# Kernel optimization log

Hardware: AMD Instinct MI355X
Metric: run time of the kernel (lower is better)

Reference implementation:

```python
import math
import jax, jax.numpy as jnp
import numpy as np

B, T_BI, D_BI = 64, 3000, 128
T_SW, D_SW = 375, 192
T_S1, D_S1 = 188, 192
N_FIRES = 300          # static fire count (target_lengths all = 300 -> beta = 1, ceil(sum)=300)
D_MODEL = 512
SCALE = 4.0            # scale_factor
EPS_LN = 1e-5


def _cif_integrate(h, alpha, thr, n_fires):
    """Vectorized CIF: cumsum + two scatter-adds (matches torch _cif_forward).
    h [B,T,D], alpha [B,T], thr [B,1] -> [B,n_fires,D]."""
    Bq, T, D = h.shape
    a = alpha / thr                       # normalize so boundaries sit at integers
    c = jnp.cumsum(a, axis=1)
    prev = c - a
    kp = jnp.floor(prev)
    kc = jnp.floor(c)
    fired = kc > kp                       # frame crosses a token boundary
    w_hi = jnp.where(fired, (c - kc) * thr, 0.0)          # leftover into new token
    w_lo = jnp.where(fired, (kp + 1.0 - prev) * thr, alpha)  # portion completing old token
    ip = jnp.clip(kp.astype(jnp.int32), 0, n_fires - 1)
    ic = jnp.clip(kc.astype(jnp.int32), 0, n_fires - 1)
    bidx = jnp.broadcast_to(jnp.arange(Bq)[:, None], (Bq, T))
    out = jnp.zeros((Bq, n_fires, D), h.dtype)
    out = out.at[bidx, ip].add(w_lo[..., None] * h)
    out = out.at[bidx, ic].add(w_hi[..., None] * h)
    return out


def _interp(src, t_cont, t_bi):
    """Linear interp of src [B,Ts,D] at continuous fire times t_cont [B,N] (given on the T_bi grid)."""
    Bq, Ts, D = src.shape
    t = t_cont * Ts / t_bi
    lo = jnp.clip(t.astype(jnp.int32), 0, Ts - 2)
    w = (t - lo.astype(t.dtype))[..., None]
    idx_lo = jnp.broadcast_to(lo[..., None], (Bq, t.shape[1], D))
    g_lo = jnp.take_along_axis(src, idx_lo, axis=1)
    g_hi = jnp.take_along_axis(src, idx_lo + 1, axis=1)
    return (1.0 - w) * g_lo + w * g_hi


def _forward(fire_signal, acoustic_src, acoustic_src_s1, conv_w, ln_g, ln_b, wp_w, wp_b,
             film_s0_w, film_s0_b, film_s1_w, film_s1_b, tproj_w, tproj_b,
             aproj_w, aproj_b, bproj_w, bproj_b, target_lengths):
    Bq, T_bi, _ = fire_signal.shape
    # 1) weight predictor: depthwise conv (k=1, no bias) -> LN -> Linear -> sigmoid
    x = fire_signal * conv_w                                   # depthwise 1x1 conv
    mu = jnp.mean(x, axis=-1, keepdims=True)
    var = jnp.var(x, axis=-1, keepdims=True)
    xn = (x - mu) * jax.lax.rsqrt(var + EPS_LN) * ln_g + ln_b
    alpha = SCALE * jax.nn.sigmoid(xn @ wp_w + wp_b)           # [B,T]
    tgt = target_lengths.astype(alpha.dtype)
    qty_loss = jnp.mean(jnp.abs(jnp.sum(alpha, axis=1) - tgt))
    # training-mode alpha normalization (sum alpha_cif == target)
    sum_a = jnp.clip(jnp.sum(alpha, axis=1, keepdims=True), 1e-8)
    alpha_cif = alpha * (tgt[:, None] / sum_a)
    # dynamic threshold beta = sum / ceil(sum)  (== 1 here since targets are integers)
    sum_cif = jnp.sum(alpha_cif, axis=1)
    ceil_sum = jax.lax.stop_gradient(jnp.clip(jnp.ceil(sum_cif), 1.0))
    thr = (sum_cif / ceil_sum)[:, None]                        # [B,1]
    # 2) CIF integration of temporal channel
    acoustic_temporal = _cif_integrate(fire_signal, alpha_cif, thr, N_FIRES)  # [B,N,128]
    # continuous fire times
    cum = jnp.cumsum(alpha_cif, axis=1)
    thresholds = jnp.arange(1, N_FIRES + 1, dtype=alpha.dtype)[None, :] * thr  # [B,N]
    ff = jax.vmap(jnp.searchsorted)(cum, thresholds)
    ff = jnp.minimum(ff, T_bi - 1)
    t_lo = jnp.maximum(ff - 1, 0)
    cum_at = jnp.take_along_axis(cum, t_lo, axis=1)
    a_at = jnp.take_along_axis(alpha_cif, ff, axis=1)
    t_cont = t_lo.astype(alpha.dtype) + (thresholds - cum_at) / jnp.clip(a_at, 1e-8)
    t_cont = jnp.clip(t_cont, 0.0, T_bi - 1)
    # 3) S0 pitch channel: interp + FiLM
    acoustic_pitch = _interp(acoustic_src, t_cont, T_bi)       # [B,N,192]
    film0 = acoustic_temporal @ film_s0_w + film_s0_b
    g0, b0 = jnp.split(film0, 2, axis=-1)
    pitch_mod = g0 * acoustic_pitch + b0
    # 4) project + combine
    embs = (acoustic_temporal @ tproj_w + tproj_b) + (pitch_mod @ aproj_w + aproj_b)
    # S1 beat channel
    acoustic_beat = _interp(acoustic_src_s1, t_cont, T_bi)     # [B,N,192]
    film1 = acoustic_temporal @ film_s1_w + film_s1_b
    g1, b1 = jnp.split(film1, 2, axis=-1)
    beat_mod = g1 * acoustic_beat + b1
    embs = embs + (beat_mod @ bproj_w + bproj_b)
    return embs, alpha, qty_loss


def setup_inputs() -> dict:
    key = jax.random.key(0)
    ks = jax.random.split(key, 14)
    # weight_proj bias init per module: alpha_init = target_fires/encoder_len
    p = min((128.0 / 3000.0) / SCALE, 0.99)
    wp_bias = math.log(p / (1.0 - p))
    f32 = jnp.float32
    return {
        "fire_signal": jax.random.normal(ks[0], (B, T_BI, D_BI), f32),
        "acoustic_src": jax.random.normal(ks[1], (B, T_SW, D_SW), f32),
        "acoustic_src_s1": jax.random.normal(ks[2], (B, T_S1, D_S1), f32),
        "target_lengths": jnp.full((B,), N_FIRES, jnp.int32),
        "conv_w": 1.0 + 0.1 * jax.random.normal(ks[3], (D_BI,), f32),
        "ln_g": jnp.ones((D_BI,), f32),
        "ln_b": jnp.zeros((D_BI,), f32),
        "wp_w": 0.02 * jax.random.normal(ks[4], (D_BI,), f32),
        "wp_b": jnp.asarray(wp_bias, f32),
        "film_s0_w": 0.02 * jax.random.normal(ks[5], (D_BI, 2 * D_SW), f32),
        "film_s0_b": jnp.concatenate([jnp.ones((D_SW,), f32), jnp.zeros((D_SW,), f32)]),
        "film_s1_w": 0.02 * jax.random.normal(ks[6], (D_BI, 2 * D_S1), f32),
        "film_s1_b": jnp.concatenate([jnp.ones((D_S1,), f32), jnp.zeros((D_S1,), f32)]),
        "tproj_w": 0.02 * jax.random.normal(ks[7], (D_BI, D_MODEL), f32),
        "tproj_b": jnp.zeros((D_MODEL,), f32),
        "aproj_w": 0.02 * jax.random.normal(ks[8], (D_SW, D_MODEL), f32),
        "aproj_b": jnp.zeros((D_MODEL,), f32),
        "bproj_w": 0.02 * jax.random.normal(ks[9], (D_S1, D_MODEL), f32),
        "bproj_b": jnp.zeros((D_MODEL,), f32),
    }


def reference(fire_signal, acoustic_src, acoustic_src_s1, target_lengths, conv_w, ln_g, ln_b,
              wp_w, wp_b, film_s0_w, film_s0_b, film_s1_w, film_s1_b, tproj_w, tproj_b,
              aproj_w, aproj_b, bproj_w, bproj_b):
    return _forward(fire_signal, acoustic_src, acoustic_src_s1, conv_w, ln_g, ln_b, wp_w, wp_b,
                    film_s0_w, film_s0_b, film_s1_w, film_s1_b, tproj_w, tproj_b,
                    aproj_w, aproj_b, bproj_w, bproj_b, target_lengths)
```

## Files before the change

### kernel.cpp

```cpp
#include <hip/hip_runtime.h>
#include <math.h>

#define BQ 64
#define TBI 3000
#define DBI 128
#define TSW 375
#define TS1 188
#define DSW 192
#define NF 300
#define DMODEL 512
#define EPSLN 1e-5f

typedef __bf16 bf16x8 __attribute__((ext_vector_type(8)));
typedef float f32x4 __attribute__((ext_vector_type(4)));

__device__ __forceinline__ unsigned short f2bf(float f) {
    unsigned u = __float_as_uint(f);
    unsigned r = (u + 0x7FFFu + ((u >> 16) & 1u)) >> 16;
    return (unsigned short)r;
}

#define ALPHA_BLOCKS 24000

__global__ __launch_bounds__(256) void k_alpha_prep(
    const float* __restrict__ fs, const float* __restrict__ conv_w,
    const float* __restrict__ ln_g, const float* __restrict__ ln_b,
    const float* __restrict__ wp_w, const float* __restrict__ wp_b,
    float* __restrict__ alpha_out,
    const float* __restrict__ f0w, const float* __restrict__ f1w,
    const float* __restrict__ tw, const float* __restrict__ aw, const float* __restrict__ bw,
    const float* __restrict__ f0b, const float* __restrict__ f1b,
    const float* __restrict__ tb, const float* __restrict__ apb, const float* __restrict__ bpb,
    unsigned short* __restrict__ Wg, unsigned short* __restrict__ Wb,
    unsigned short* __restrict__ W2,
    float* __restrict__ gbias, float* __restrict__ bbias, float* __restrict__ bias2,
    float* __restrict__ qtyo)
{
    if (blockIdx.x >= ALPHA_BLOCKS) {
        int pbid = blockIdx.x - ALPHA_BLOCKS;
        if (pbid == 1216) {
            for (int c = threadIdx.x; c < 512; c += 256) {
                if (c < 384) {
                    gbias[c] = c < 192 ? f0b[c] : f1b[c - 192];
                    bbias[c] = c < 192 ? f0b[c + 192] : f1b[c - 192 + 192];
                }
                bias2[c] = tb[c] + apb[c] + bpb[c];
            }
            if (threadIdx.x == 0) qtyo[0] = 0.f;
            return;
        }
        int i = pbid * 256 + threadIdx.x;
        if (i < 49152) {
            int k = i / 384;
            int n = i - k * 384;
            float g, b;
            if (n < 192) { g = f0w[k * 384 + n]; b = f0w[k * 384 + n + 192]; }
            else         { g = f1w[k * 384 + (n - 192)]; b = f1w[k * 384 + n]; }
            int kt = k >> 5, j = k & 7;
            int lane = ((k >> 3) & 3) * 16 + (n & 15);
            int nt = n >> 4;
            int out = ((nt * 4 + kt) * 64 + lane) * 8 + j;
            Wg[out] = f2bf(g); Wb[out] = f2bf(b);
        } else {
            int ii = i - 49152;
            int k = ii >> 9, n = ii & 511;
            float v;
            if (k < 128)      v = tw[k * 512 + n];
            else if (k < 320) v = aw[(k - 128) * 512 + n];
            else              v = bw[(k - 320) * 512 + n];
            int kt = k >> 5, j = k & 7;
            int lane = ((k >> 3) & 3) * 16 + (n & 15);
            int nt = n >> 4;
            int out = ((nt * 16 + kt) * 64 + lane) * 8 + j;
            W2[out] = f2bf(v);
        }
        return;
    }
    int wave = threadIdx.x >> 6, lane = threadIdx.x & 63;
    int l = lane & 31;
    long g = (long)blockIdx.x * 8 + wave * 2 + (lane >> 5);
    const float* row = fs + g * DBI;
    float4 f  = *(const float4*)&row[4 * l];
    float4 cw = *(const float4*)&conv_w[4 * l];
    float4 x; x.x = f.x * cw.x; x.y = f.y * cw.y; x.z = f.z * cw.z; x.w = f.w * cw.w;
    float s = x.x + x.y + x.z + x.w;
    for (int m = 16; m >= 1; m >>= 1) s += __shfl_xor(s, m, 64);
    float mu = s * (1.0f / 128.0f);
    float4 d; d.x = x.x - mu; d.y = x.y - mu; d.z = x.z - mu; d.w = x.w - mu;
    float q = d.x * d.x + d.y * d.y + d.z * d.z + d.w * d.w;
    for (int m = 16; m >= 1; m >>= 1) q += __shfl_xor(q, m, 64);
    float var = q * (1.0f / 128.0f);
    float rs = rsqrtf(var + EPSLN);
    float4 lg = *(const float4*)&ln_g[4 * l];
    float4 lb = *(const float4*)&ln_b[4 * l];
    float4 wp = *(const float4*)&wp_w[4 * l];
    float z = (d.x * rs * lg.x + lb.x) * wp.x + (d.y * rs * lg.y + lb.y) * wp.y
            + (d.z * rs * lg.z + lb.z) * wp.z + (d.w * rs * lg.w + lb.w) * wp.w;
    for (int m = 16; m >= 1; m >>= 1) z += __shfl_xor(z, m, 64);
    z += wp_b[0];
    float a = 4.0f / (1.0f + expf(-z));
    if (l == 0) alpha_out[g] = a;
}

__global__ __launch_bounds__(1024) void k_scan4(
    const float* __restrict__ alpha, const int* __restrict__ tlen,
    float2* __restrict__ params, float* __restrict__ qtyo,
    float2* __restrict__ c2, float* __restrict__ tcont, int* __restrict__ ffout)
{
    __shared__ float2 sc[TBI];
    __shared__ float2 part[2][1024];
    __shared__ double wpart[16];
    int b = blockIdx.x, tid = threadIdx.x;
    int wv = tid >> 6, ln = tid & 63;
    const float* ar = alpha + (long)b * TBI;
    double s = 0.0;
    for (int t = tid; t < TBI; t += 1024) s += (double)ar[t];
    for (int m = 32; m >= 1; m >>= 1) s += __shfl_xor(s, m, 64);
    if (ln == 0) wpart[wv] = s;
    __syncthreads();
    if (wv == 0) {
        double d = (ln < 16) ? wpart[ln] : 0.0;
        for (int m = 8; m >= 1; m >>= 1) d += __shfl_xor(d, m, 64);
        if (ln == 0) wpart[0] = d;
    }
    __syncthreads();
    double sum_a = wpart[0];
    __syncthreads();
    double tgt = (double)tlen[b];
    double sa = sum_a < 1e-8 ? 1e-8 : sum_a;
    float r = (float)(tgt / sa);
    double s2 = 0.0;
    for (int t = tid; t < TBI; t += 1024) s2 += (double)(ar[t] * r);
    for (int m = 32; m >= 1; m >>= 1) s2 += __shfl_xor(s2, m, 64);
    if (ln == 0) wpart[wv] = s2;
    __syncthreads();
    if (wv == 0) {
        double d = (ln < 16) ? wpart[ln] : 0.0;
        for (int m = 8; m >= 1; m >>= 1) d += __shfl_xor(d, m, 64);
        if (ln == 0) wpart[0] = d;
    }
    __syncthreads();
    float sum_cif = (float)wpart[0];
    float cs = ceilf(sum_cif); if (cs < 1.0f) cs = 1.0f;
    float thr = sum_cif / cs;
    float rthr = 1.0f / thr;
    if (tid == 0) {
        params[b] = make_float2(r, thr);
        atomicAdd(qtyo, (float)fabs(sum_a - tgt) * (1.0f / (float)BQ));
    }
    int base = tid * 3;
    float2 run = make_float2(0.f, 0.f);
    if (base < TBI) {
        for (int j = 0; j < 3; ++j) {
            int t = base + j;
            float ac = ar[t] * r;
            run.x += ac * rthr; run.y += ac;
            sc[t] = run;
        }
    }
    part[0][tid] = (base < TBI) ? run : make_float2(0.f, 0.f);
    __syncthreads();
    int srcb = 0;
    for (int d = 1; d < 1024; d <<= 1) {
        float2 v = part[srcb][tid];
        if (tid >= d) { float2 u = part[srcb][tid - d]; v.x += u.x; v.y += u.y; }
        part[srcb ^ 1][tid] = v;
        srcb ^= 1;
        __syncthreads();
    }
    if (base < TBI && tid > 0) {
        float2 off = part[srcb][tid - 1];
        for (int j = 0; j < 3; ++j) { sc[base + j].x += off.x; sc[base + j].y += off.y; }
    }
    __syncthreads();
    for (int t = tid; t < TBI; t += 1024) {
        float ac = ar[t] * r;
        c2[(long)b * TBI + t] = make_float2(sc[t].x, ac);
    }
    if (tid < NF) {
        float v = (float)(tid + 1) * thr;
        int lo = 0, hi = TBI;
        while (lo < hi) { int mid = (lo + hi) >> 1; if (sc[mid].y < v) lo = mid + 1; else hi = mid; }
        int ff = lo; if (ff > TBI - 1) ff = TBI - 1;
        ffout[b * NF + tid] = ff;
        int tl = ff - 1; if (tl < 0) tl = 0;
        float cum_at = sc[tl].y;
        float a_at = ar[ff] * r;
        if (a_at < 1e-8f) a_at = 1e-8f;
        float tc = (float)tl + (v - cum_at) / a_at;
        tc = fminf(fmaxf(tc, 0.0f), (float)(TBI - 1));
        tcont[b * NF + tid] = tc;
    }
}

__global__ __launch_bounds__(256) void k_cif5(
    const float* __restrict__ fs, const float2* __restrict__ c2,
    const int* __restrict__ ffA, const float2* __restrict__ params,
    unsigned short* __restrict__ at)
{
    int wid = threadIdx.x >> 6, lane = threadIdx.x & 63;
    int wg = blockIdx.x * 4 + wid;
    int b = wg / NF, j = wg - b * NF;
    const int* ffb = ffA + b * NF;
    int s = (j == 0) ? 0 : ffb[j - 1];
    int e = (j == NF - 1) ? (TBI - 1) : ffb[j];
    float thr = params[b].y;
    float rthr = 1.0f / thr;
    const float2* cb = c2 + (long)b * TBI;
    const float* fb = fs + (long)b * TBI * DBI;
    float a0 = 0.f, a1 = 0.f;
    #define CIF_BODY(T) do { \
        float2 v = cb[T]; \
        float2 h = *(const float2*)&fb[(long)(T) * DBI + 2 * lane]; \
        float c = v.x, ac = v.y; \
        float av = ac * rthr; \
        float prev = c - av; \
        float kp = floorf(prev), kc = floorf(c); \
        bool fired = kc > kp; \
        float w_lo = fired ? (kp + 1.0f - prev) * thr : ac; \
        float w_hi = fired ? (c - kc) * thr : 0.0f; \
        int ip = (int)kp; if (ip > NF - 1) ip = NF - 1; if (ip < 0) ip = 0; \
        int ic = (int)kc; if (ic > NF - 1) ic = NF - 1; if (ic < 0) ic = 0; \
        if (ip == j) { a0 += w_lo * h.x; a1 += w_lo * h.y; } \
        if (fired && ic == j) { a0 += w_hi * h.x; a1 += w_hi * h.y; } \
    } while (0)
    int t = s;
    for (; t + 1 <= e; t += 2) { CIF_BODY(t); CIF_BODY(t + 1); }
    if (t <= e) CIF_BODY(t);
    #undef CIF_BODY
    unsigned short* ab = at + (long)b * NF * DBI;
    *(unsigned*)&ab[j * DBI + 2 * lane] = (unsigned)f2bf(a0) | ((unsigned)f2bf(a1) << 16);
}

#define EROWS 32
__global__ __launch_bounds__(256, 4) void k_emb11(
    const unsigned short* __restrict__ atb, const float* __restrict__ tcont,
    const float* __restrict__ src0, const float* __restrict__ src1,
    const unsigned short* __restrict__ Wg, const unsigned short* __restrict__ Wb,
    const unsigned short* __restrict__ W2,
    const float* __restrict__ gbias, const float* __restrict__ bbias,
    const float* __restrict__ bias2, float* __restrict__ embs)
{
    __shared__ __align__(16) unsigned short X[EROWS][520];
    __shared__ float s_w0[EROWS], s_w1[EROWS];
    __shared__ int s_lo0[EROWS], s_lo1[EROWS], s_b[EROWS];
    int tid = threadIdx.x;
    int wave = tid >> 6, lane = tid & 63;
    long r0 = (long)blockIdx.x * EROWS;
    for (int idx = tid; idx < 512; idx += 256) {
        int r = idx >> 4, k8 = (idx & 15) * 8;
        *(uint4*)&X[r][k8] = *(const uint4*)&atb[(r0 + r) * DBI + k8];
    }
    if (tid < EROWS) {
        long g = r0 + tid;
        s_b[tid] = (int)(g / NF);
        float tc = tcont[g];
        float t0 = tc * ((float)TSW / 3000.0f);
        int lo0 = (int)t0; if (lo0 > TSW - 2) lo0 = TSW - 2; if (lo0 < 0) lo0 = 0;
        s_lo0[tid] = lo0; s_w0[tid] = t0 - (float)lo0;
        float t1 = tc * ((float)TS1 / 3000.0f);
        int lo1 = (int)t1; if (lo1 > TS1 - 2) lo1 = TS1 - 2; if (lo1 < 0) lo1 = 0;
        s_lo1[tid] = lo1; s_w1[tid] = t1 - (float)lo1;
    }
    __syncthreads();
    int mrow = lane & 15, quad = lane >> 4;
    for (int i = 0; i < 6; ++i) {
        int nt = wave + 4 * i;
        f32x4 ag0 = {0,0,0,0}, ab0 = {0,0,0,0}, ag1 = {0,0,0,0}, ab1 = {0,0,0,0};
        #pragma unroll
        for (int kt = 0; kt < 4; ++kt) {
            bf16x8 a0 = *(const bf16x8*)&X[mrow][kt * 32 + quad * 8];
            bf16x8 a1 = *(const bf16x8*)&X[mrow + 16][kt * 32 + quad * 8];
            bf16x8 bg = *(const bf16x8*)&Wg[(((nt * 4 + kt) * 64) + lane) * 8];
            bf16x8 bb = *(const bf16x8*)&Wb[(((nt * 4 + kt) * 64) + lane) * 8];
            ag0 = __builtin_amdgcn_mfma_f32_16x16x32_bf16(a0, bg, ag0, 0, 0, 0);
            ab0 = __builtin_amdgcn_mfma_f32_16x16x32_bf16(a0, bb, ab0, 0, 0, 0);
            ag1 = __builtin_amdgcn_mfma_f32_16x16x32_bf16(a1, bg, ag1, 0, 0, 0);
            ab1 = __builtin_amdgcn_mfma_f32_16x16x32_bf16(a1, bb, ab1, 0, 0, 0);
        }
        int c = nt * 16 + mrow;
        bool sel = c >= DSW;
        int cc = sel ? c - DSW : c;
        const float* S = sel ? src1 : src0;
        int Ts = sel ? TS1 : TSW;
        float gb = gbias[c], bbv = bbias[c];
        #pragma unroll
        for (int q = 0; q < 4; ++q) {
            {
                int r = quad * 4 + q;
                int b = s_b[r];
                int lo = sel ? s_lo1[r] : s_lo0[r];
                float w = sel ? s_w1[r] : s_w0[r];
                const float* Sp = S + ((long)b * Ts + lo) * DSW + cc;
                float pv = (1.0f - w) * Sp[0] + w * Sp[DSW];
                X[r][128 + c] = f2bf((ag0[q] + gb) * pv + (ab0[q] + bbv));
            }
            {
                int r = quad * 4 + q + 16;
                int b = s_b[r];
                int lo = sel ? s_lo1[r] : s_lo0[r];
                float w = sel ? s_w1[r] : s_w0[r];
                const float* Sp = S + ((long)b * Ts + lo) * DSW + cc;
                float pv = (1.0f - w) * Sp[0] + w * Sp[DSW];
                X[r][128 + c] = f2bf((ag1[q] + gb) * pv + (ab1[q] + bbv));
            }
        }
    }
    __syncthreads();
    f32x4 acc[2][8];
    #pragma unroll
    for (int h = 0; h < 2; ++h)
        #pragma unroll
        for (int n = 0; n < 8; ++n) acc[h][n] = (f32x4){0, 0, 0, 0};
    for (int kt = 0; kt < 16; ++kt) {
        bf16x8 a0 = *(const bf16x8*)&X[mrow][kt * 32 + quad * 8];
        bf16x8 a1 = *(const bf16x8*)&X[mrow + 16][kt * 32 + quad * 8];
        #pragma unroll
        for (int n = 0; n < 8; ++n) {
            int nt = wave * 8 + n;
            bf16x8 bfv = *(const bf16x8*)&W2[((nt * 16 + kt) * 64 + lane) * 8];
            acc[0][n] = __builtin_amdgcn_mfma_f32_16x16x32_bf16(a0, bfv, acc[0][n], 0, 0, 0);
            acc[1][n] = __builtin_amdgcn_mfma_f32_16x16x32_bf16(a1, bfv, acc[1][n], 0, 0, 0);
        }
    }
    #pragma unroll
    for (int n = 0; n < 8; ++n) {
        int cbase = (wave * 8 + n) * 16 + mrow;
        float bv = bias2[cbase];
        #pragma unroll
        for (int q = 0; q < 4; ++q) {
            embs[(r0 + quad * 4 + q) * DMODEL + cbase] = acc[0][n][q] + bv;
            embs[(r0 + 16 + quad * 4 + q) * DMODEL + cbase] = acc[1][n][q] + bv;
        }
    }
}

extern "C" void kernel_launch(void* const* d_in, const int* in_sizes, int n_in,
                              void* d_out, int out_size, void* d_ws, size_t ws_size,
                              hipStream_t stream)
{
    const float* fs     = (const float*)d_in[0];
    const float* src0   = (const float*)d_in[1];
    const float* src1   = (const float*)d_in[2];
    const int*   tlen   = (const int*)d_in[3];
    const float* conv_w = (const float*)d_in[4];
    const float* ln_g   = (const float*)d_in[5];
    const float* ln_b   = (const float*)d_in[6];
    const float* wp_w   = (const float*)d_in[7];
    const float* wp_b   = (const float*)d_in[8];
    const float* f0w    = (const float*)d_in[9];
    const float* f0b    = (const float*)d_in[10];
    const float* f1w    = (const float*)d_in[11];
    const float* f1b    = (const float*)d_in[12];
    const float* tw     = (const float*)d_in[13];
    const float* tb     = (const float*)d_in[14];
    const float* aw     = (const float*)d_in[15];
    const float* apb    = (const float*)d_in[16];
    const float* bw     = (const float*)d_in[17];
    const float* bpb    = (const float*)d_in[18];

    float* embs  = (float*)d_out;
    float* alpha = embs + (long)BQ * NF * DMODEL;
    float* qtyo  = alpha + (long)BQ * TBI;

    char* ws = (char*)d_ws;
    size_t off = 0;
    unsigned short* at = (unsigned short*)(ws + off); off += 4915200;
    float2* c2     = (float2*)(ws + off); off += 1536000;
    float*  tcont  = (float*)(ws + off);  off += 76800;
    int*    ffA    = (int*)(ws + off);    off += 76800;
    float2* params = (float2*)(ws + off); off += 512;
    unsigned short* Wg = (unsigned short*)(ws + off); off += 98304;
    unsigned short* Wb = (unsigned short*)(ws + off); off += 98304;
    unsigned short* W2 = (unsigned short*)(ws + off); off += 524288;
    float* gbias = (float*)(ws + off); off += 1536;
    float* bbias = (float*)(ws + off); off += 1536;
    float* bias2 = (float*)(ws + off); off += 2048;

    k_alpha_prep<<<ALPHA_BLOCKS + 1217, 256, 0, stream>>>(
        fs, conv_w, ln_g, ln_b, wp_w, wp_b, alpha,
        f0w, f1w, tw, aw, bw, f0b, f1b, tb, apb, bpb,
        Wg, Wb, W2, gbias, bbias, bias2, qtyo);
    k_scan4<<<BQ, 1024, 0, stream>>>(alpha, tlen, params, qtyo, c2, tcont, ffA);
    k_cif5<<<(BQ * NF) / 4, 256, 0, stream>>>(fs, c2, ffA, params, at);
    k_emb11<<<(BQ * NF) / EROWS, 256, 0, stream>>>(at, tcont, src0, src1,
                                                   Wg, Wb, W2, gbias, bbias, bias2, embs);
}
```

Before: 280.9 us.

## Split fused FiLM+projection kernel into separate FiLM and GEMM kernels

Breaks the single embedding kernel into two. The first computes the FiLM-modulated interpolated features for 16-row tiles and writes them as bf16 to a global workspace. The second reloads those features with the CIF tokens and runs the final 512-wide projection GEMM. The aim is to let each stage pick its own tile size and occupancy, at the cost of an extra launch and a round trip of about 15 MB through global memory.

```diff
diff --git a/kernel.cpp b/kernel.cpp
--- a/kernel.cpp
+++ b/kernel.cpp
@@ -232,26 +232,25 @@
     *(unsigned*)&ab[j * DBI + 2 * lane] = (unsigned)f2bf(a0) | ((unsigned)f2bf(a1) << 16);
 }
 
-#define EROWS 32
-__global__ __launch_bounds__(256, 4) void k_emb11(
+#define FROWS 16
+__global__ __launch_bounds__(256, 4) void k_film(
     const unsigned short* __restrict__ atb, const float* __restrict__ tcont,
     const float* __restrict__ src0, const float* __restrict__ src1,
     const unsigned short* __restrict__ Wg, const unsigned short* __restrict__ Wb,
-    const unsigned short* __restrict__ W2,
     const float* __restrict__ gbias, const float* __restrict__ bbias,
-    const float* __restrict__ bias2, float* __restrict__ embs)
-{
-    __shared__ __align__(16) unsigned short X[EROWS][520];
-    __shared__ float s_w0[EROWS], s_w1[EROWS];
-    __shared__ int s_lo0[EROWS], s_lo1[EROWS], s_b[EROWS];
+    unsigned short* __restrict__ Xg)
+{
+    __shared__ __align__(16) unsigned short X[FROWS][136];
+    __shared__ float s_w0[FROWS], s_w1[FROWS];
+    __shared__ int s_lo0[FROWS], s_lo1[FROWS], s_b[FROWS];
     int tid = threadIdx.x;
     int wave = tid >> 6, lane = tid & 63;
-    long r0 = (long)blockIdx.x * EROWS;
-    for (int idx = tid; idx < 512; idx += 256) {
-        int r = idx >> 4, k8 = (idx & 15) * 8;
+    long r0 = (long)blockIdx.x * FROWS;
+    {
+        int r = tid >> 4, k8 = (tid & 15) * 8;
         *(uint4*)&X[r][k8] = *(const uint4*)&atb[(r0 + r) * DBI + k8];
     }
-    if (tid < EROWS) {
+    if (tid < FROWS) {
         long g = r0 + tid;
         s_b[tid] = (int)(g / NF);
         float tc = tcont[g];
@@ -266,17 +265,14 @@
     int mrow = lane & 15, quad = lane >> 4;
     for (int i = 0; i < 6; ++i) {
         int nt = wave + 4 * i;
-        f32x4 ag0 = {0,0,0,0}, ab0 = {0,0,0,0}, ag1 = {0,0,0,0}, ab1 = {0,0,0,0};
+        f32x4 ag0 = {0,0,0,0}, ab0 = {0,0,0,0};
         #pragma unroll
         for (int kt = 0; kt < 4; ++kt) {
             bf16x8 a0 = *(const bf16x8*)&X[mrow][kt * 32 + quad * 8];
-            bf16x8 a1 = *(const bf16x8*)&X[mrow + 16][kt * 32 + quad * 8];
             bf16x8 bg = *(const bf16x8*)&Wg[(((nt * 4 + kt) * 64) + lane) * 8];
             bf16x8 bb = *(const bf16x8*)&Wb[(((nt * 4 + kt) * 64) + lane) * 8];
             ag0 = __builtin_amdgcn_mfma_f32_16x16x32_bf16(a0, bg, ag0, 0, 0, 0);
             ab0 = __builtin_amdgcn_mfma_f32_16x16x32_bf16(a0, bb, ab0, 0, 0, 0);
-            ag1 = __builtin_amdgcn_mfma_f32_16x16x32_bf16(a1, bg, ag1, 0, 0, 0);
-            ab1 = __builtin_amdgcn_mfma_f32_16x16x32_bf16(a1, bb, ab1, 0, 0, 0);
         }
         int c = nt * 16 + mrow;
         bool sel = c >= DSW;
@@ -286,27 +282,37 @@
         float gb = gbias[c], bbv = bbias[c];
         #pragma unroll
         for (int q = 0; q < 4; ++q) {
-            {
-                int r = quad * 4 + q;
-                int b = s_b[r];
-                int lo = sel ? s_lo1[r] : s_lo0[r];
-                float w = sel ? s_w1[r] : s_w0[r];
-                const float* Sp = S + ((long)b * Ts + lo) * DSW + cc;
-                float pv = (1.0f - w) * Sp[0] + w * Sp[DSW];
-                X[r][128 + c] = f2bf((ag0[q] + gb) * pv + (ab0[q] + bbv));
-            }
-            {
-                int r = quad * 4 + q + 16;
-                int b = s_b[r];
-                int lo = sel ? s_lo1[r] : s_lo0[r];
-                float w = sel ? s_w1[r] : s_w0[r];
-                const float* Sp = S + ((long)b * Ts + lo) * DSW + cc;
-                float pv = (1.0f - w) * Sp[0] + w * Sp[DSW];
-                X[r][128 + c] = f2bf((ag1[q] + gb) * pv + (ab1[q] + bbv));
-            }
-        }
-    }
-    __syncthreads();
+            int r = quad * 4 + q;
+            int b = s_b[r];
+            int lo = sel ? s_lo1[r] : s_lo0[r];
+            float w = sel ? s_w1[r] : s_w0[r];
+            const float* Sp = S + ((long)b * Ts + lo) * DSW + cc;
+            float pv = (1.0f - w) * Sp[0] + w * Sp[DSW];
+            Xg[(r0 + r) * 384 + c] = f2bf((ag0[q] + gb) * pv + (ab0[q] + bbv));
+        }
+    }
+}
+
+#define EROWS 32
+__global__ __launch_bounds__(256, 3) void k_gemm2(
+    const unsigned short* __restrict__ atb, const unsigned short* __restrict__ Xg,
+    const unsigned short* __restrict__ W2, const float* __restrict__ bias2,
+    float* __restrict__ embs)
+{
+    __shared__ __align__(16) unsigned short X[EROWS][520];
+    int tid = threadIdx.x;
+    int wave = tid >> 6, lane = tid & 63;
+    long r0 = (long)blockIdx.x * EROWS;
+    for (int idx = tid; idx < 512; idx += 256) {
+        int r = idx >> 4, k8 = (idx & 15) * 8;
+        *(uint4*)&X[r][k8] = *(const uint4*)&atb[(r0 + r) * DBI + k8];
+    }
+    for (int idx = tid; idx < 1536; idx += 256) {
+        int r = idx / 48, c8 = (idx - r * 48) * 8;
+        *(uint4*)&X[r][128 + c8] = *(const uint4*)&Xg[(r0 + r) * 384 + c8];
+    }
+    __syncthreads();
+    int mrow = lane & 15, quad = lane >> 4;
     f32x4 acc[2][8];
     #pragma unroll
     for (int h = 0; h < 2; ++h)
@@ -376,6 +382,7 @@
     float* gbias = (float*)(ws + off); off += 1536;
     float* bbias = (float*)(ws + off); off += 1536;
     float* bias2 = (float*)(ws + off); off += 2048;
+    unsigned short* Xg = (unsigned short*)(ws + off); off += 14745600;
 
     k_alpha_prep<<<ALPHA_BLOCKS + 1217, 256, 0, stream>>>(
         fs, conv_w, ln_g, ln_b, wp_w, wp_b, alpha,
@@ -383,6 +390,7 @@
         Wg, Wb, W2, gbias, bbias, bias2, qtyo);
     k_scan4<<<BQ, 1024, 0, stream>>>(alpha, tlen, params, qtyo, c2, tcont, ffA);
     k_cif5<<<(BQ * NF) / 4, 256, 0, stream>>>(fs, c2, ffA, params, at);
-    k_emb11<<<(BQ * NF) / EROWS, 256, 0, stream>>>(at, tcont, src0, src1,
-                                                   Wg, Wb, W2, gbias, bbias, bias2, embs);
-}
+    k_film<<<(BQ * NF) / FROWS, 256, 0, stream>>>(at, tcont, src0, src1,
+                                                  Wg, Wb, gbias, bbias, Xg);
+    k_gemm2<<<(BQ * NF) / EROWS, 256, 0, stream>>>(at, Xg, W2, bias2, embs);
+}
```

Measured after the change: 286.0 us. About the same (+1.8%).
